# Kernel optimization log

Hardware: AMD Instinct MI355X
Metric: run time of the kernel (lower is better)

## Reference

```python
import jax, jax.numpy as jnp
import numpy as np

FACTORS = (16, 8, 8)          # prod == n_embd == 1024
H, DK = 16, 64
FACTOR_PARAMS = tuple(f * (f - 1) // 2 for f in FACTORS)  # (120, 28, 28)
DV = sum(FACTOR_PARAMS)       # 176
DVP = 256                     # next power of two padding
B, T, C = 2, 2048, 1024
OFFSET = 64


def _skew_exp(params, f):
    """params: (..., f*(f-1)//2) -> rotation matrices (..., f, f) via expm of skew-sym."""
    rows, cols = np.triu_indices(f, k=1)
    batch = params.shape[:-1]
    mat = jnp.zeros(batch + (f, f), jnp.float32).at[..., rows, cols].set(params.astype(jnp.float32))
    S = mat - jnp.swapaxes(mat, -1, -2)
    R = jax.vmap(jax.scipy.linalg.expm)(S.reshape((-1, f, f)))
    return R.reshape(batch + (f, f))


def setup_inputs() -> dict:
    key = jax.random.key(0)
    k1, k2, k3, k4, k5 = jax.random.split(key, 5)
    return {
        "x": jax.random.normal(k1, (B, T, C), jnp.float32),
        "cached_k": jax.random.normal(k2, (B, H, OFFSET, DK), jnp.float32),
        "cached_v": jax.random.normal(k3, (B, H, OFFSET, DVP), jnp.float32),
        "W_QK": jax.random.normal(k4, (2 * H * DK, C), jnp.float32) * 0.02,
        "W_V": jax.random.normal(k5, (H * DV, C), jnp.float32) * 0.02,
    }


def reference(x, cached_k, cached_v, W_QK, W_V):
    Bx, Tx, Cx = x.shape
    qk = x @ W_QK.T                                  # (B,T,2*H*DK)
    q, k = jnp.split(qk, 2, axis=-1)
    q = q.reshape(Bx, Tx, H, DK).transpose(0, 2, 1, 3)   # (B,H,T,DK)
    k = k.reshape(Bx, Tx, H, DK).transpose(0, 2, 1, 3)
    v = (x @ W_V.T).reshape(Bx, Tx, H, DV).transpose(0, 2, 1, 3)  # (B,H,T,DV)
    v = jnp.pad(v, ((0, 0), (0, 0), (0, 0), (0, DVP - DV)))       # pad to DVP

    offset = cached_k.shape[2]
    k = jnp.concatenate([cached_k, k], axis=2)       # (B,H,offset+T,DK)
    v = jnp.concatenate([cached_v, v], axis=2)       # (B,H,offset+T,DVP)

    neg_inf = jnp.finfo(jnp.float32).min
    causal = jnp.triu(jnp.full((Tx, Tx), neg_inf, jnp.float32), k=1)
    mask = jnp.concatenate([jnp.zeros((Tx, offset), jnp.float32), causal], axis=1)

    scores = jnp.einsum('bhqd,bhkd->bhqk', q, k) * (1.0 / np.sqrt(DK)) + mask
    attn = jax.nn.softmax(scores, axis=-1)
    rot = jnp.einsum('bhqk,bhkd->bhqd', attn, v)[..., :DV]   # (B,H,T,DV)
    rot = rot.transpose(0, 2, 1, 3).sum(axis=2)              # sum over heads -> (B,T,DV)

    splits = jnp.split(rot, np.cumsum(FACTOR_PARAMS)[:-1].tolist(), axis=-1)
    y = x.reshape(Bx, Tx, *FACTORS)
    for i, (p, f) in enumerate(zip(splits, FACTORS)):
        R = _skew_exp(p, f).astype(x.dtype)          # (B,T,f,f)
        y = jnp.moveaxis(y, 2 + i, 2)
        sh = y.shape
        y = (R @ y.reshape(Bx, Tx, f, -1)).reshape(sh)
        y = jnp.moveaxis(y, 2, 2 + i)
    y = y.reshape(Bx, Tx, Cx)
    return y, k, v
```

## Files before the change

kernel.cpp:

```cpp
#include <hip/hip_runtime.h>

typedef _Float16 h8 __attribute__((ext_vector_type(8)));
typedef _Float16 h4 __attribute__((ext_vector_type(4)));
typedef float f4 __attribute__((ext_vector_type(4)));

#define NB 2
#define NT 2048
#define NC 1024
#define NH 16
#define DKK 64
#define DV 176
#define DVP 256
#define OFF 64
#define KV 2112
#define SCALE_Q 0.18033688011112f
#define CLAMP_S 11.541560327111f

__device__ __forceinline__ void load_lds16(const _Float16* g, _Float16* l) {
    __builtin_amdgcn_global_load_lds(
        (const __attribute__((address_space(1))) void*)g,
        (__attribute__((address_space(3))) void*)l, 16, 0, 0);
}

#define PREPA_X   1048576
#define PREPA_QK  1572864
#define PREPA_WV  2293760
#define PREPA_END 2473984
__global__ __launch_bounds__(256)
void k_prep_a(const float* __restrict__ x, const float* __restrict__ wqk,
              const float* __restrict__ wv, _Float16* __restrict__ xh,
              _Float16* __restrict__ wqkh, _Float16* __restrict__ wvh,
              float* __restrict__ rotb) {
    int i = blockIdx.x * 256 + threadIdx.x;
    if (i >= PREPA_END) return;
    if (i < PREPA_X) {
        float4 v = *(const float4*)(x + (size_t)i * 4);
        h4 h = {(_Float16)v.x, (_Float16)v.y, (_Float16)v.z, (_Float16)v.w};
        *(h4*)(xh + (size_t)i * 4) = h;
    } else if (i < PREPA_QK) {
        int j = i - PREPA_X;
        float4 v = *(const float4*)(wqk + (size_t)j * 4);
        h4 h = {(_Float16)v.x, (_Float16)v.y, (_Float16)v.z, (_Float16)v.w};
        *(h4*)(wqkh + (size_t)j * 4) = h;
    } else if (i < PREPA_WV) {
        int j = i - PREPA_QK;
        float4 v = *(const float4*)(wv + (size_t)j * 4);
        h4 h = {(_Float16)v.x, (_Float16)v.y, (_Float16)v.z, (_Float16)v.w};
        *(h4*)(wvh + (size_t)j * 4) = h;
    } else {
        int j = i - PREPA_WV;
        *(float4*)(rotb + (size_t)j * 4) = (float4){0.f, 0.f, 0.f, 0.f};
    }
}

#define PREPB_CK   32768
#define PREPB_CV   163840
#define PREPB_END  1474560
__global__ __launch_bounds__(256)
void k_prep_b(const float* __restrict__ ck, const float* __restrict__ cv,
              float* __restrict__ out_k, _Float16* __restrict__ kh,
              float* __restrict__ out_v, _Float16* __restrict__ vTh) {
    int i = blockIdx.x * 256 + threadIdx.x;
    if (i >= PREPB_END) return;
    if (i < PREPB_CK) {
        int bh = i >> 10, rem = i & 1023;
        int pos = rem >> 4, d4 = (rem & 15) * 4;
        float4 v = *(const float4*)(ck + (size_t)i * 4);
        size_t o = ((size_t)bh * KV + pos) * DKK + d4;
        *(float4*)(out_k + o) = v;
        h4 h = {(_Float16)v.x, (_Float16)v.y, (_Float16)v.z, (_Float16)v.w};
        *(h4*)(kh + o) = h;
    } else if (i < PREPB_CV) {
        int j = i - PREPB_CK;
        int bh = j >> 12, rem = j & 4095;
        int pos = rem >> 6, c4 = (rem & 63) * 4;
        float4 v = *(const float4*)(cv + (size_t)j * 4);
        *(float4*)(out_v + ((size_t)bh * KV + pos) * DVP + c4) = v;
        if (c4 < DV) {
            _Float16* vt = vTh + ((size_t)bh * DV + c4) * KV + pos;
            vt[0]              = (_Float16)v.x;
            vt[KV]             = (_Float16)v.y;
            vt[2 * (size_t)KV] = (_Float16)v.z;
            vt[3 * (size_t)KV] = (_Float16)v.w;
        }
    } else {
        int j = i - PREPB_CV;
        int bh = j / 40960, rem = j - bh * 40960;
        int t = rem / 20, c4 = DV + (rem - t * 20) * 4;
        *(float4*)(out_v + ((size_t)bh * KV + OFF + t) * DVP + c4) = (float4){0.f, 0.f, 0.f, 0.f};
    }
}

__global__ __launch_bounds__(256)
void k_gemm_fused(const _Float16* __restrict__ xh, const _Float16* __restrict__ wh,
                  _Float16* __restrict__ qh, _Float16* __restrict__ kh,
                  float* __restrict__ out_k, _Float16* __restrict__ vTh,
                  float* __restrict__ out_v) {
    __shared__ char smem_raw[65536];
    auto Ts = (_Float16(*)[64][72])smem_raw;
    auto Tq = (_Float16(*)[128][68])smem_raw;

    const int tid = threadIdx.x;
    const int lane = tid & 63, w = tid >> 6;
    const int lr = lane & 15, lg = lane >> 4;
    const int wm = w >> 1, wn = w & 1;
    const int n = blockIdx.x, x = n & 7, idx = n >> 3;
    const int c_  = idx >> 6;
    const int loc = idx & 63;
    const int mi = (x & 3) * 8 + (loc & 7);
    const int ni = (x >> 2) * 19 + c_ * 8 + (loc >> 3);
    const int m0 = mi * 128, n0 = ni * 128;
    const int srow = lane >> 3;
    const int sc16 = (lane & 7) ^ srow;

    f4 acc[4][4];
#pragma unroll
    for (int i = 0; i < 4; i++)
#pragma unroll
        for (int j = 0; j < 4; j++) acc[i][j] = (f4){0.f, 0.f, 0.f, 0.f};

    auto stage = [&](int buf, int k0) {
        _Float16* Ab = (_Float16*)smem_raw + buf * 8192;
        _Float16* Bb = (_Float16*)(smem_raw + 32768) + buf * 8192;
#pragma unroll
        for (int j = 0; j < 4; j++) {
            int i = w * 4 + j;
            int row = i * 8 + srow;
            load_lds16(&xh[(size_t)(m0 + row) * NC + k0 + sc16 * 8], Ab + i * 512);
            load_lds16(&wh[(size_t)(n0 + row) * NC + k0 + sc16 * 8], Bb + i * 512);
        }
    };

    stage(0, 0);
    int cur = 0;
    for (int t = 0; t < 16; ++t) {
        if (t < 15) {
            stage(cur ^ 1, (t + 1) * 64);
            asm volatile("s_waitcnt vmcnt(8)" ::: "memory");
        } else {
            asm volatile("s_waitcnt vmcnt(0)" ::: "memory");
        }
        __builtin_amdgcn_s_barrier();
        __builtin_amdgcn_sched_barrier(0);

        const _Float16* Ab = (const _Float16*)smem_raw + cur * 8192;
        const _Float16* Bb = (const _Float16*)(smem_raw + 32768) + cur * 8192;
#pragma unroll
        for (int ks = 0; ks < 2; ks++) {
            h8 a[4], b[4];
#pragma unroll
            for (int mt = 0; mt < 4; mt++) {
                int row = wm * 64 + mt * 16 + lr;
                a[mt] = *(const h8*)&Ab[row * 64 + ((ks * 4 + lg) ^ (lr & 7)) * 8];
            }
#pragma unroll
            for (int nt = 0; nt < 4; nt++) {
                int row = wn * 64 + nt * 16 + lr;
                b[nt] = *(const h8*)&Bb[row * 64 + ((ks * 4 + lg) ^ (lr & 7)) * 8];
            }
            __builtin_amdgcn_s_setprio(1);
#pragma unroll
            for (int mt = 0; mt < 4; mt++)
#pragma unroll
                for (int nt = 0; nt < 4; nt++)
                    acc[mt][nt] = __builtin_amdgcn_mfma_f32_16x16x32_f16(a[mt], b[nt], acc[mt][nt], 0, 0, 0);
            __builtin_amdgcn_s_setprio(0);
        }
        __builtin_amdgcn_sched_barrier(0);
        __builtin_amdgcn_s_barrier();
        cur ^= 1;
    }

    const int b_ = m0 >> 11;
    const int mloc = m0 & (NT - 1);

    if (ni < 8) {
        __syncthreads();
#pragma unroll
        for (int mt = 0; mt < 4; mt++)
#pragma unroll
            for (int nt = 0; nt < 4; nt++)
#pragma unroll
                for (int r = 0; r < 4; r++)
                    Tq[wn][wm * 64 + mt * 16 + lg * 4 + r][nt * 16 + lr] =
                        (_Float16)(acc[mt][nt][r] * SCALE_Q);
        __syncthreads();
        const int h0 = n0 >> 6;
#pragma unroll
        for (int i = 0; i < 8; i++) {
            int id = i * 256 + tid;
            int hh = id >> 10, rem = id & 1023;
            int t = rem >> 3, dk8 = (rem & 7) * 8;
            h8 v = *(const h8*)&Tq[hh][t][dk8];
            *(h8*)&qh[((size_t)(b_ * NH + h0 + hh) * NT + mloc + t) * DKK + dk8] = v;
        }
    } else if (ni < 16) {
        __syncthreads();
#pragma unroll
        for (int mt = 0; mt < 4; mt++)
#pragma unroll
            for (int nt = 0; nt < 4; nt++)
#pragma unroll
                for (int r = 0; r < 4; r++) {
                    int t = wm * 64 + mt * 16 + lg * 4 + r;
                    int g2 = n0 - 1024 + wn * 64 + nt * 16 + lr;
                    float v = acc[mt][nt][r];
                    int h = g2 >> 6, dk = g2 & 63;
                    out_k[((size_t)(b_ * NH + h) * KV + OFF + mloc + t) * DKK + dk] = v;
                    Tq[wn][t][nt * 16 + lr] = (_Float16)v;
                }
        __syncthreads();
        const int h0 = (n0 - 1024) >> 6;
#pragma unroll
        for (int i = 0; i < 8; i++) {
            int id = i * 256 + tid;
            int hh = id >> 10, rem = id & 1023;
            int t = rem >> 3, dk8 = (rem & 7) * 8;
            h8 v = *(const h8*)&Tq[hh][t][dk8];
            *(h8*)&kh[((size_t)(b_ * NH + h0 + hh) * KV + OFF + mloc + t) * DKK + dk8] = v;
        }
    } else {
        __syncthreads();
#pragma unroll
        for (int mt = 0; mt < 4; mt++)
#pragma unroll
            for (int nt = 0; nt < 4; nt++) {
                h4 ph;
#pragma unroll
                for (int r = 0; r < 4; r++) {
                    int grow = m0 + wm * 64 + mt * 16 + lg * 4 + r;
                    int gcol = n0 - 2048 + wn * 64 + nt * 16 + lr;
                    float v = acc[mt][nt][r];
                    int bb = grow >> 11, t = grow & (NT - 1);
                    int h = gcol / DV;
                    int c = gcol - h * DV;
                    out_v[((size_t)(bb * NH + h) * KV + OFF + t) * DVP + c] = v;
                    ph[r] = (_Float16)v;
                }
                *(h4*)&Ts[w][nt * 16 + lr][mt * 16 + lg * 4] = ph;
            }
        __syncthreads();
        {
            _Float16* vout = vTh + ((size_t)b_ * (NH * DV) + (n0 - 2048)) * KV + OFF + mloc;
            const int seg = tid & 31;
            const int rr = tid >> 5;
#pragma unroll
            for (int i = 0; i < 16; i++) {
                int c = i * 8 + rr;
                int buf = ((seg >> 4) << 1) | (c >> 6);
                h4 vv = *(const h4*)&Ts[buf][c & 63][(seg & 15) * 4];
                *(h4*)&vout[(size_t)c * KV + seg * 4] = vv;
            }
        }
    }
}

__global__ __launch_bounds__(256, 4)
void k_attn(const _Float16* __restrict__ qh, const _Float16* __restrict__ kh,
            const _Float16* __restrict__ vTh, float* __restrict__ rot) {
    __shared__ _Float16 Ks[64][64];
    __shared__ _Float16 Vs[176][64];
    __shared__ _Float16 Ps[4][16][72];
    const int tid = threadIdx.x, lane = tid & 63, w = tid >> 6;
    const int lr = lane & 15, lg = lane >> 4;
    const int n = blockIdx.x;
    const int gq = 31 - (n >> 5);
    const int bh = (n & 7) + 8 * ((n >> 3) & 3);
    const int b_ = bh >> 4;
    const int qt = gq * 4 + w;
    const int q = qt * 16 + lr;

    const _Float16* qp = qh + ((size_t)bh * NT + q) * DKK;
    h8 bq0 = *(const h8*)(qp + lg * 8);
    h8 bq1 = *(const h8*)(qp + 32 + lg * 8);

    const _Float16* kbase = kh + (size_t)bh * KV * DKK;
    const _Float16* vbase = vTh + (size_t)bh * DV * KV;

    f4 o[11];
#pragma unroll
    for (int i = 0; i < 11; i++) o[i] = (f4){0.f, 0.f, 0.f, 0.f};
    float l_acc = 0.f;

    const int nkt = gq + 2;
    const int srow = lane >> 3, sslot = lane & 7;
    const int sc16 = sslot ^ srow;

    for (int kt = 0; kt < nkt; kt++) {
        __syncthreads();
#pragma unroll
        for (int j = 0; j < 2; j++) {
            int i = w * 2 + j;
            int row = i * 8 + srow;
            load_lds16(&kbase[(size_t)(kt * 64 + row) * DKK + sc16 * 8],
                       (_Float16*)Ks + i * 512);
        }
#pragma unroll
        for (int j = 0; j < 6; j++) {
            int i = w * 6 + j;
            if (i < 22) {
                int row = i * 8 + srow;
                load_lds16(&vbase[(size_t)row * KV + kt * 64 + sc16 * 8],
                           (_Float16*)Vs + i * 512);
            }
        }
        asm volatile("s_waitcnt vmcnt(0)" ::: "memory");
        __syncthreads();

        f4 s[4];
        __builtin_amdgcn_s_setprio(1);
#pragma unroll
        for (int nt = 0; nt < 4; nt++) {
            int krow = nt * 16 + lr;
            h8 ak0 = *(const h8*)&Ks[krow][(lg ^ (lr & 7)) * 8];
            h8 ak1 = *(const h8*)&Ks[krow][((4 + lg) ^ (lr & 7)) * 8];
            f4 st = (f4){0.f, 0.f, 0.f, 0.f};
            st = __builtin_amdgcn_mfma_f32_16x16x32_f16(ak0, bq0, st, 0, 0, 0);
            st = __builtin_amdgcn_mfma_f32_16x16x32_f16(ak1, bq1, st, 0, 0, 0);
            s[nt] = st;
        }
        __builtin_amdgcn_s_setprio(0);

        if (kt + 1 < nkt) {
#pragma unroll
            for (int nt = 0; nt < 4; nt++) {
                h4 ph;
#pragma unroll
                for (int r = 0; r < 4; r++) {
                    float p = __builtin_exp2f(fminf(s[nt][r], CLAMP_S));
                    l_acc += p;
                    ph[r] = (_Float16)p;
                }
                *(h4*)&Ps[w][lr][nt * 16 + lg * 4] = ph;
            }
        } else {
#pragma unroll
            for (int nt = 0; nt < 4; nt++) {
                h4 ph;
#pragma unroll
                for (int r = 0; r < 4; r++) {
                    int key = kt * 64 + nt * 16 + lg * 4 + r;
                    float sv = fminf(s[nt][r], CLAMP_S);
                    float p = (key <= q + OFF) ? __builtin_exp2f(sv) : 0.f;
                    l_acc += p;
                    ph[r] = (_Float16)p;
                }
                *(h4*)&Ps[w][lr][nt * 16 + lg * 4] = ph;
            }
        }

        __builtin_amdgcn_s_setprio(1);
#pragma unroll
        for (int ks = 0; ks < 2; ks++) {
            h8 ap = *(const h8*)&Ps[w][lr][ks * 32 + lg * 8];
#pragma unroll
            for (int nt = 0; nt < 11; nt++) {
                int vrow = nt * 16 + lr;
                h8 bv = *(const h8*)&Vs[vrow][((ks * 4 + lg) ^ (lr & 7)) * 8];
                o[nt] = __builtin_amdgcn_mfma_f32_16x16x32_f16(ap, bv, o[nt], 0, 0, 0);
            }
        }
        __builtin_amdgcn_s_setprio(0);
    }

    l_acc += __shfl_xor(l_acc, 16);
    l_acc += __shfl_xor(l_acc, 32);
    float lq[4];
#pragma unroll
    for (int r = 0; r < 4; r++) lq[r] = 1.f / __shfl(l_acc, lg * 4 + r);
#pragma unroll
    for (int r = 0; r < 4; r++) {
        int t = qt * 16 + lg * 4 + r;
#pragma unroll
        for (int nt = 0; nt < 11; nt++) {
            atomicAdd(&rot[((size_t)b_ * NT + t) * DV + nt * 16 + lr], o[nt][r] * lq[r]);
        }
    }
}

__device__ __forceinline__ int triu16(int r, int c) { return r * 15 - (r * (r - 1)) / 2 + (c - r - 1); }
__device__ __forceinline__ int triu8(int r, int c)  { return r * 7  - (r * (r - 1)) / 2 + (c - r - 1); }

__global__ __launch_bounds__(64)
void k_rotate(const float* __restrict__ x, const float* __restrict__ rot,
              float* __restrict__ y) {
    __shared__ float A16[16][16], Ta[16][16], Tb[16][16];
    __shared__ float A8[2][8][8], T8a[2][8][8], T8b[2][8][8];
    __shared__ float pbuf[176];
    __shared__ float xt[1024], t1[1024], t2[1024];
    const int tok = blockIdx.x;
    const int lane = threadIdx.x;

    for (int i = lane; i < 176; i += 64) pbuf[i] = rot[(size_t)tok * DV + i];
    for (int i = lane; i < 1024; i += 64) xt[i] = x[(size_t)tok * NC + i];
    __syncthreads();

#pragma unroll
    for (int j = 0; j < 4; j++) {
        int e = lane * 4 + j, r = e >> 4, c = e & 15;
        float v = 0.f;
        if (r < c) v = pbuf[triu16(r, c)];
        else if (r > c) v = -pbuf[triu16(c, r)];
        A16[r][c] = v;
    }
    {
        int r = lane >> 3, c = lane & 7;
#pragma unroll
        for (int m = 0; m < 2; m++) {
            float v = 0.f;
            if (r < c) v = pbuf[120 + m * 28 + triu8(r, c)];
            else if (r > c) v = -pbuf[120 + m * 28 + triu8(c, r)];
            A8[m][r][c] = v;
        }
    }
    __syncthreads();

    float rn = 0.f;
    if (lane < 16) {
#pragma unroll
        for (int c = 0; c < 16; c++) rn += fabsf(A16[lane][c]);
    }
#pragma unroll
    for (int mm = 1; mm < 16; mm <<= 1) rn = fmaxf(rn, __shfl_xor(rn, mm));
    rn = __shfl(rn, 0);
    int s = 0;
    while (rn > 0.5f && s < 60) { rn *= 0.5f; s++; }
    const float sc16 = exp2f((float)(-s));
    __syncthreads();
#pragma unroll
    for (int j = 0; j < 4; j++) { int e = lane * 4 + j; A16[e >> 4][e & 15] *= sc16; }
    __syncthreads();
#pragma unroll
    for (int j = 0; j < 4; j++) {
        int e = lane * 4 + j, r = e >> 4, c = e & 15;
        Ta[r][c] = (r == c ? 1.f : 0.f) + A16[r][c] * (1.f / 12.f);
    }
    __syncthreads();
    float (*Tc)[16] = Ta, (*Tn)[16] = Tb;
    for (int k = 11; k >= 1; k--) {
#pragma unroll
        for (int j = 0; j < 4; j++) {
            int e = lane * 4 + j, r = e >> 4, c = e & 15;
            float acc = 0.f;
#pragma unroll
            for (int q = 0; q < 16; q++) acc += A16[r][q] * Tc[q][c];
            Tn[r][c] = acc * (1.f / (float)k) + (r == c ? 1.f : 0.f);
        }
        __syncthreads();
        float (*tmp)[16] = Tc; Tc = Tn; Tn = tmp;
    }
    for (int it = 0; it < s; it++) {
#pragma unroll
        for (int j = 0; j < 4; j++) {
            int e = lane * 4 + j, r = e >> 4, c = e & 15;
            float acc = 0.f;
#pragma unroll
            for (int q = 0; q < 16; q++) acc += Tc[r][q] * Tc[q][c];
            Tn[r][c] = acc;
        }
        __syncthreads();
        float (*tmp)[16] = Tc; Tc = Tn; Tn = tmp;
    }

    float (*R2p)[8] = T8a[0];
    float (*R3p)[8] = T8a[1];
    {
        int r = lane >> 3, c = lane & 7;
        for (int m = 0; m < 2; m++) {
            float rn8 = 0.f;
            if (lane < 8) {
#pragma unroll
                for (int cc = 0; cc < 8; cc++) rn8 += fabsf(A8[m][lane][cc]);
            }
#pragma unroll
            for (int mm = 1; mm < 8; mm <<= 1) rn8 = fmaxf(rn8, __shfl_xor(rn8, mm));
            rn8 = __shfl(rn8, 0);
            int s8 = 0;
            while (rn8 > 0.5f && s8 < 60) { rn8 *= 0.5f; s8++; }
            float sc8 = exp2f((float)(-s8));
            __syncthreads();
            A8[m][r][c] *= sc8;
            __syncthreads();
            T8a[m][r][c] = (r == c ? 1.f : 0.f) + A8[m][r][c] * (1.f / 12.f);
            __syncthreads();
            float (*tc)[8] = T8a[m], (*tn)[8] = T8b[m];
            for (int k = 11; k >= 1; k--) {
                float acc = 0.f;
#pragma unroll
                for (int q = 0; q < 8; q++) acc += A8[m][r][q] * tc[q][c];
                tn[r][c] = acc * (1.f / (float)k) + (r == c ? 1.f : 0.f);
                __syncthreads();
                float (*tmp)[8] = tc; tc = tn; tn = tmp;
            }
            for (int it = 0; it < s8; it++) {
                float acc = 0.f;
#pragma unroll
                for (int q = 0; q < 8; q++) acc += tc[r][q] * tc[q][c];
                tn[r][c] = acc;
                __syncthreads();
                float (*tmp)[8] = tc; tc = tn; tn = tmp;
            }
            if (m == 0) R2p = tc; else R3p = tc;
        }
    }
    __syncthreads();

    for (int o = lane; o < 1024; o += 64) {
        int c = o & 7, base = o & ~7;
        float acc = 0.f;
#pragma unroll
        for (int j = 0; j < 8; j++) acc += R3p[c][j] * xt[base + j];
        t1[o] = acc;
    }
    __syncthreads();
    for (int o = lane; o < 1024; o += 64) {
        int c = o & 7, bb = (o >> 3) & 7, a = o >> 6;
        float acc = 0.f;
#pragma unroll
        for (int j = 0; j < 8; j++) acc += R2p[bb][j] * t1[a * 64 + j * 8 + c];
        t2[o] = acc;
    }
    __syncthreads();
    for (int o = lane; o < 1024; o += 64) {
        int rr = o & 63, a = o >> 6;
        float acc = 0.f;
#pragma unroll
        for (int j = 0; j < 16; j++) acc += Tc[a][j] * t2[j * 64 + rr];
        y[(size_t)tok * NC + o] = acc;
    }
}

extern "C" void kernel_launch(void* const* d_in, const int* in_sizes, int n_in,
                              void* d_out, int out_size, void* d_ws, size_t ws_size,
                              hipStream_t stream) {
    const float* x   = (const float*)d_in[0];
    const float* ck  = (const float*)d_in[1];
    const float* cv  = (const float*)d_in[2];
    const float* wqk = (const float*)d_in[3];
    const float* wv  = (const float*)d_in[4];

    float* out_y = (float*)d_out;
    float* out_k = out_y + (size_t)NB * NT * NC;
    float* out_v = out_k + (size_t)NB * NH * KV * DKK;

    char* ws = (char*)d_ws;
    _Float16* xh   = (_Float16*)ws;  ws += (size_t)NB * NT * NC * 2;
    _Float16* wqkh = (_Float16*)ws;  ws += (size_t)2 * NH * DKK * NC * 2;
    _Float16* wvh  = (_Float16*)ws;  ws += (size_t)NH * DV * NC * 2;
    _Float16* qh   = (_Float16*)ws;  ws += (size_t)NB * NH * NT * DKK * 2;
    _Float16* kh   = (_Float16*)ws;  ws += (size_t)NB * NH * KV * DKK * 2;
    _Float16* vTh  = (_Float16*)ws;  ws += (size_t)NB * NH * DV * KV * 2;
    float*    rotb = (float*)ws;     ws += (size_t)NB * NT * DV * 4;

    k_prep_a<<<dim3((PREPA_END + 255) / 256), dim3(256), 0, stream>>>(
        x, wqk, wv, xh, wqkh, wvh, rotb);
    k_prep_b<<<dim3((PREPB_END + 255) / 256), dim3(256), 0, stream>>>(
        ck, cv, out_k, kh, out_v, vTh);

    k_gemm_fused<<<dim3(1216), dim3(256), 0, stream>>>(xh, wqkh, qh, kh, out_k, vTh, out_v);

    k_attn<<<dim3(1024), dim3(256), 0, stream>>>(qh, kh, vTh, rotb);

    k_rotate<<<dim3(NB * NT), dim3(64), 0, stream>>>(x, rotb, out_y);
}
```

Before: 176.7 us.

## Double-buffer K/V tiles in attention and merge matrix-exponential passes

```diff
diff --git a/kernel.cpp b/kernel.cpp
--- a/kernel.cpp
+++ b/kernel.cpp
@@ -255,11 +255,11 @@
     }
 }
 
-__global__ __launch_bounds__(256, 4)
+__global__ __launch_bounds__(256, 2)
 void k_attn(const _Float16* __restrict__ qh, const _Float16* __restrict__ kh,
             const _Float16* __restrict__ vTh, float* __restrict__ rot) {
-    __shared__ _Float16 Ks[64][64];
-    __shared__ _Float16 Vs[176][64];
+    __shared__ _Float16 Ks[2][64][64];
+    __shared__ _Float16 Vs[2][176][64];
     __shared__ _Float16 Ps[4][16][72];
     const int tid = threadIdx.x, lane = tid & 63, w = tid >> 6;
     const int lr = lane & 15, lg = lane >> 4;
@@ -286,34 +286,44 @@
     const int srow = lane >> 3, sslot = lane & 7;
     const int sc16 = sslot ^ srow;
 
+    auto stage = [&](int buf, int kt) {
+#pragma unroll
+        for (int t = 0; t < 8; t++) {
+            int i = w * 8 + t;
+            if (i > 29) i = 29;
+            if (i < 8) {
+                int row = i * 8 + srow;
+                load_lds16(&kbase[(size_t)(kt * 64 + row) * DKK + sc16 * 8],
+                           (_Float16*)Ks[buf] + i * 512);
+            } else {
+                int j = i - 8;
+                int row = j * 8 + srow;
+                load_lds16(&vbase[(size_t)row * KV + kt * 64 + sc16 * 8],
+                           (_Float16*)Vs[buf] + j * 512);
+            }
+        }
+    };
+
+    stage(0, 0);
+    int cur = 0;
+
     for (int kt = 0; kt < nkt; kt++) {
-        __syncthreads();
-#pragma unroll
-        for (int j = 0; j < 2; j++) {
-            int i = w * 2 + j;
-            int row = i * 8 + srow;
-            load_lds16(&kbase[(size_t)(kt * 64 + row) * DKK + sc16 * 8],
-                       (_Float16*)Ks + i * 512);
-        }
-#pragma unroll
-        for (int j = 0; j < 6; j++) {
-            int i = w * 6 + j;
-            if (i < 22) {
-                int row = i * 8 + srow;
-                load_lds16(&vbase[(size_t)row * KV + kt * 64 + sc16 * 8],
-                           (_Float16*)Vs + i * 512);
-            }
-        }
-        asm volatile("s_waitcnt vmcnt(0)" ::: "memory");
-        __syncthreads();
+        if (kt + 1 < nkt) {
+            stage(cur ^ 1, kt + 1);
+            asm volatile("s_waitcnt vmcnt(8)" ::: "memory");
+        } else {
+            asm volatile("s_waitcnt vmcnt(0)" ::: "memory");
+        }
+        __builtin_amdgcn_s_barrier();
+        __builtin_amdgcn_sched_barrier(0);
 
         f4 s[4];
         __builtin_amdgcn_s_setprio(1);
 #pragma unroll
         for (int nt = 0; nt < 4; nt++) {
             int krow = nt * 16 + lr;
-            h8 ak0 = *(const h8*)&Ks[krow][(lg ^ (lr & 7)) * 8];
-            h8 ak1 = *(const h8*)&Ks[krow][((4 + lg) ^ (lr & 7)) * 8];
+            h8 ak0 = *(const h8*)&Ks[cur][krow][(lg ^ (lr & 7)) * 8];
+            h8 ak1 = *(const h8*)&Ks[cur][krow][((4 + lg) ^ (lr & 7)) * 8];
             f4 st = (f4){0.f, 0.f, 0.f, 0.f};
             st = __builtin_amdgcn_mfma_f32_16x16x32_f16(ak0, bq0, st, 0, 0, 0);
             st = __builtin_amdgcn_mfma_f32_16x16x32_f16(ak1, bq1, st, 0, 0, 0);
@@ -356,11 +366,14 @@
 #pragma unroll
             for (int nt = 0; nt < 11; nt++) {
                 int vrow = nt * 16 + lr;
-                h8 bv = *(const h8*)&Vs[vrow][((ks * 4 + lg) ^ (lr & 7)) * 8];
+                h8 bv = *(const h8*)&Vs[cur][vrow][((ks * 4 + lg) ^ (lr & 7)) * 8];
                 o[nt] = __builtin_amdgcn_mfma_f32_16x16x32_f16(ap, bv, o[nt], 0, 0, 0);
             }
         }
         __builtin_amdgcn_s_setprio(0);
+        __builtin_amdgcn_sched_barrier(0);
+        __builtin_amdgcn_s_barrier();
+        cur ^= 1;
     }
 
     l_acc += __shfl_xor(l_acc, 16);
@@ -403,14 +416,14 @@
         else if (r > c) v = -pbuf[triu16(c, r)];
         A16[r][c] = v;
     }
+    const int r8 = lane >> 3, c8 = lane & 7;
     {
-        int r = lane >> 3, c = lane & 7;
 #pragma unroll
         for (int m = 0; m < 2; m++) {
             float v = 0.f;
-            if (r < c) v = pbuf[120 + m * 28 + triu8(r, c)];
-            else if (r > c) v = -pbuf[120 + m * 28 + triu8(c, r)];
-            A8[m][r][c] = v;
+            if (r8 < c8) v = pbuf[120 + m * 28 + triu8(r8, c8)];
+            else if (r8 > c8) v = -pbuf[120 + m * 28 + triu8(c8, r8)];
+            A8[m][r8][c8] = v;
         }
     }
     __syncthreads();
@@ -423,86 +436,108 @@
 #pragma unroll
     for (int mm = 1; mm < 16; mm <<= 1) rn = fmaxf(rn, __shfl_xor(rn, mm));
     rn = __shfl(rn, 0);
-    int s = 0;
-    while (rn > 0.5f && s < 60) { rn *= 0.5f; s++; }
-    const float sc16 = exp2f((float)(-s));
-    __syncthreads();
-#pragma unroll
-    for (int j = 0; j < 4; j++) { int e = lane * 4 + j; A16[e >> 4][e & 15] *= sc16; }
+    int s16 = 0;
+    while (rn > 0.5f && s16 < 60) { rn *= 0.5f; s16++; }
+
+    int s8v[2];
+#pragma unroll
+    for (int m = 0; m < 2; m++) {
+        float rn8 = 0.f;
+        if (lane < 8) {
+#pragma unroll
+            for (int cc = 0; cc < 8; cc++) rn8 += fabsf(A8[m][lane][cc]);
+        }
+#pragma unroll
+        for (int mm = 1; mm < 8; mm <<= 1) rn8 = fmaxf(rn8, __shfl_xor(rn8, mm));
+        rn8 = __shfl(rn8, 0);
+        int s8 = 0;
+        while (rn8 > 0.5f && s8 < 60) { rn8 *= 0.5f; s8++; }
+        s8v[m] = s8;
+    }
+    const float sc16 = exp2f((float)(-s16));
+    const float sc80 = exp2f((float)(-s8v[0]));
+    const float sc81 = exp2f((float)(-s8v[1]));
+    __syncthreads();
+
+#pragma unroll
+    for (int j = 0; j < 4; j++) {
+        int e = lane * 4 + j, r = e >> 4, c = e & 15;
+        A16[r][c] *= sc16;
+    }
+    A8[0][r8][c8] *= sc80;
+    A8[1][r8][c8] *= sc81;
     __syncthreads();
 #pragma unroll
     for (int j = 0; j < 4; j++) {
         int e = lane * 4 + j, r = e >> 4, c = e & 15;
         Ta[r][c] = (r == c ? 1.f : 0.f) + A16[r][c] * (1.f / 12.f);
     }
-    __syncthreads();
+    T8a[0][r8][c8] = (r8 == c8 ? 1.f : 0.f) + A8[0][r8][c8] * (1.f / 12.f);
+    T8a[1][r8][c8] = (r8 == c8 ? 1.f : 0.f) + A8[1][r8][c8] * (1.f / 12.f);
+    __syncthreads();
+
     float (*Tc)[16] = Ta, (*Tn)[16] = Tb;
+    float (*tc0)[8] = T8a[0], (*tn0)[8] = T8b[0];
+    float (*tc1)[8] = T8a[1], (*tn1)[8] = T8b[1];
+
     for (int k = 11; k >= 1; k--) {
+        float inv_k = 1.f / (float)k;
 #pragma unroll
         for (int j = 0; j < 4; j++) {
             int e = lane * 4 + j, r = e >> 4, c = e & 15;
             float acc = 0.f;
 #pragma unroll
-            for (int q = 0; q < 16; q++) acc += A16[r][q] * Tc[q][c];
-            Tn[r][c] = acc * (1.f / (float)k) + (r == c ? 1.f : 0.f);
-        }
-        __syncthreads();
-        float (*tmp)[16] = Tc; Tc = Tn; Tn = tmp;
-    }
-    for (int it = 0; it < s; it++) {
-#pragma unroll
-        for (int j = 0; j < 4; j++) {
-            int e = lane * 4 + j, r = e >> 4, c = e & 15;
-            float acc = 0.f;
-#pragma unroll
-            for (int q = 0; q < 16; q++) acc += Tc[r][q] * Tc[q][c];
-            Tn[r][c] = acc;
-        }
-        __syncthreads();
-        float (*tmp)[16] = Tc; Tc = Tn; Tn = tmp;
-    }
-
-    float (*R2p)[8] = T8a[0];
-    float (*R3p)[8] = T8a[1];
-    {
-        int r = lane >> 3, c = lane & 7;
-        for (int m = 0; m < 2; m++) {
-            float rn8 = 0.f;
-            if (lane < 8) {
-#pragma unroll
-                for (int cc = 0; cc < 8; cc++) rn8 += fabsf(A8[m][lane][cc]);
-            }
-#pragma unroll
-            for (int mm = 1; mm < 8; mm <<= 1) rn8 = fmaxf(rn8, __shfl_xor(rn8, mm));
-            rn8 = __shfl(rn8, 0);
-            int s8 = 0;
-            while (rn8 > 0.5f && s8 < 60) { rn8 *= 0.5f; s8++; }
-            float sc8 = exp2f((float)(-s8));
-            __syncthreads();
-            A8[m][r][c] *= sc8;
-            __syncthreads();
-            T8a[m][r][c] = (r == c ? 1.f : 0.f) + A8[m][r][c] * (1.f / 12.f);
-            __syncthreads();
-            float (*tc)[8] = T8a[m], (*tn)[8] = T8b[m];
-            for (int k = 11; k >= 1; k--) {
+            for (int qv = 0; qv < 16; qv++) acc += A16[r][qv] * Tc[qv][c];
+            Tn[r][c] = acc * inv_k + (r == c ? 1.f : 0.f);
+        }
+        {
+            float a0 = 0.f, a1 = 0.f;
+#pragma unroll
+            for (int qv = 0; qv < 8; qv++) {
+                a0 += A8[0][r8][qv] * tc0[qv][c8];
+                a1 += A8[1][r8][qv] * tc1[qv][c8];
+            }
+            tn0[r8][c8] = a0 * inv_k + (r8 == c8 ? 1.f : 0.f);
+            tn1[r8][c8] = a1 * inv_k + (r8 == c8 ? 1.f : 0.f);
+        }
+        __syncthreads();
+        { float (*t)[16] = Tc; Tc = Tn; Tn = t; }
+        { float (*t)[8] = tc0; tc0 = tn0; tn0 = t; }
+        { float (*t)[8] = tc1; tc1 = tn1; tn1 = t; }
+    }
+
+    int smax = s16 > s8v[0] ? s16 : s8v[0];
+    if (s8v[1] > smax) smax = s8v[1];
+    for (int it = 0; it < smax; it++) {
+        if (it < s16) {
+#pragma unroll
+            for (int j = 0; j < 4; j++) {
+                int e = lane * 4 + j, r = e >> 4, c = e & 15;
                 float acc = 0.f;
 #pragma unroll
-                for (int q = 0; q < 8; q++) acc += A8[m][r][q] * tc[q][c];
-                tn[r][c] = acc * (1.f / (float)k) + (r == c ? 1.f : 0.f);
-                __syncthreads();
-                float (*tmp)[8] = tc; tc = tn; tn = tmp;
-            }
-            for (int it = 0; it < s8; it++) {
-                float acc = 0.f;
-#pragma unroll
-                for (int q = 0; q < 8; q++) acc += tc[r][q] * tc[q][c];
-                tn[r][c] = acc;
-                __syncthreads();
-                float (*tmp)[8] = tc; tc = tn; tn = tmp;
-            }
-            if (m == 0) R2p = tc; else R3p = tc;
-        }
-    }
+                for (int qv = 0; qv < 16; qv++) acc += Tc[r][qv] * Tc[qv][c];
+                Tn[r][c] = acc;
+            }
+        }
+        if (it < s8v[0]) {
+            float a0 = 0.f;
+#pragma unroll
+            for (int qv = 0; qv < 8; qv++) a0 += tc0[r8][qv] * tc0[qv][c8];
+            tn0[r8][c8] = a0;
+        }
+        if (it < s8v[1]) {
+            float a1 = 0.f;
+#pragma unroll
+            for (int qv = 0; qv < 8; qv++) a1 += tc1[r8][qv] * tc1[qv][c8];
+            tn1[r8][c8] = a1;
+        }
+        __syncthreads();
+        if (it < s16) { float (*t)[16] = Tc; Tc = Tn; Tn = t; }
+        if (it < s8v[0]) { float (*t)[8] = tc0; tc0 = tn0; tn0 = t; }
+        if (it < s8v[1]) { float (*t)[8] = tc1; tc1 = tn1; tn1 = t; }
+    }
+    float (*R2p)[8] = tc0;
+    float (*R3p)[8] = tc1;
     __syncthreads();
 
     for (int o = lane; o < 1024; o += 64) {
```

Result: slower. 196.2 us (+11.1%).
